# Kernel optimization log

Measured on AMD Instinct MI355X. Metric: run time of the kernel, lower is better.

## Reference

```python
import jax, jax.numpy as jnp
import numpy as np

H = 16  # heads


def setup_inputs() -> dict:
    key = jax.random.key(0)
    ks = jax.random.split(key, 10)
    B, S, M = 4, 2048, 1024
    scale = 1.0 / np.sqrt(M)
    return {
        "x": jax.random.normal(ks[0], (B, S, M), dtype=jnp.float32),
        "mask": jax.random.uniform(ks[1], (B, 1, S, S), dtype=jnp.float32),
        "Wq": jax.random.normal(ks[2], (M, M), dtype=jnp.float32) * scale,
        "bq": jax.random.normal(ks[3], (M,), dtype=jnp.float32) * scale,
        "Wk": jax.random.normal(ks[4], (M, M), dtype=jnp.float32) * scale,
        "bk": jax.random.normal(ks[5], (M,), dtype=jnp.float32) * scale,
        "Wv": jax.random.normal(ks[6], (M, M), dtype=jnp.float32) * scale,
        "bv": jax.random.normal(ks[7], (M,), dtype=jnp.float32) * scale,
        "Wo": jax.random.normal(ks[8], (M, M), dtype=jnp.float32) * scale,
        "bo": jax.random.normal(ks[9], (M,), dtype=jnp.float32) * scale,
    }


def reference(x, mask, Wq, bq, Wk, bk, Wv, bv, Wo, bo):
    B, S, M = x.shape
    dk = M // H
    # QKV projections (torch Linear: x @ W.T + b), then split heads -> [B,H,S,dk]
    q = (x @ Wq.T + bq).reshape(B, S, H, dk).transpose(0, 2, 1, 3)
    k = (x @ Wk.T + bk).reshape(B, S, H, dk).transpose(0, 2, 1, 3)
    v = (x @ Wv.T + bv).reshape(B, S, H, dk).transpose(0, 2, 1, 3)
    # scores: [B,H,S,S], multiplicative mask (non-standard!) then softmax
    scores = jnp.einsum("bhqd,bhkd->bhqk", q, k) / jnp.sqrt(jnp.float32(dk))
    scores = scores * mask  # mask broadcasts over heads
    attn = jax.nn.softmax(scores, axis=-1)
    # dropout is identity in eval/reference mode
    out = jnp.einsum("bhqk,bhkd->bhqd", attn, v)  # [B,H,S,dk]
    concat = out.transpose(0, 2, 1, 3).reshape(B, S, M)
    return concat @ Wo.T + bo
```

## Files before the change

### kernel.cpp

```cpp
#include <hip/hip_runtime.h>

typedef __attribute__((ext_vector_type(8))) short s16x8;
typedef __attribute__((ext_vector_type(4))) short s16x4;
typedef __attribute__((ext_vector_type(4))) float f32x4;
typedef __attribute__((ext_vector_type(16))) float f32x16;
typedef __attribute__((ext_vector_type(2))) unsigned int u32x2;

#define DEV static __device__ __forceinline__

DEV void gload_lds16(const void* g, void* l) {
  __builtin_amdgcn_global_load_lds(
      (const __attribute__((address_space(1))) void*)g,
      (__attribute__((address_space(3))) void*)l, 16, 0, 0);
}

DEV unsigned short f2bf(float f) {
  unsigned int u = __float_as_uint(f);
  u = (u + 0x7fffu + ((u >> 16) & 1u)) >> 16;
  return (unsigned short)u;
}

DEV unsigned pk2(float lo, float hi) {
  unsigned r;
  asm("v_cvt_pk_bf16_f32 %0, %1, %2" : "=v"(r) : "v"(lo), "v"(hi));
  return r;
}

DEV float exp2_fast(float x) {
  float r;
  asm("v_exp_f32 %0, %1" : "=v"(r) : "v"(x));
  return r;
}

DEV void cvt8(const float* __restrict__ in, unsigned short* __restrict__ out, int i) {
  float4 a = *(const float4*)(in + i);
  float4 b = *(const float4*)(in + i + 4);
  union { s16x8 v; unsigned short u[8]; } o;
  o.u[0] = f2bf(a.x); o.u[1] = f2bf(a.y); o.u[2] = f2bf(a.z); o.u[3] = f2bf(a.w);
  o.u[4] = f2bf(b.x); o.u[5] = f2bf(b.y); o.u[6] = f2bf(b.z); o.u[7] = f2bf(b.w);
  *(s16x8*)(out + i) = o.v;
}

__global__ __launch_bounds__(256) void k_cvt_all(
    const float* __restrict__ x, const float* __restrict__ Wq,
    const float* __restrict__ Wk, const float* __restrict__ Wv,
    const float* __restrict__ Wo, unsigned short* __restrict__ xb,
    unsigned short* __restrict__ wcat) {
  const int bid = blockIdx.x;
  if (bid < 4096) {
    cvt8(x, xb, (bid * 256 + threadIdx.x) * 8);
  } else {
    const int id = bid - 4096;
    const int sel = id >> 9;
    const float* in = (sel == 0) ? Wq : (sel == 1) ? Wk : (sel == 2) ? Wv : Wo;
    cvt8(in, wcat + sel * 1048576, ((id & 511) * 256 + threadIdx.x) * 8);
  }
}

__global__ __launch_bounds__(256) void k_gemm_qkv(
    const unsigned short* __restrict__ A, const unsigned short* __restrict__ Bcat,
    const float* __restrict__ bq, const float* __restrict__ bk,
    const float* __restrict__ bv,
    unsigned short* __restrict__ outQK, unsigned short* __restrict__ vtw) {
  constexpr int K = 1024;
  constexpr float QSC = 0.125f * 1.44269504f;
  __shared__ unsigned short As[128 * 64];
  __shared__ unsigned short Bs[128 * 64];

  const int lin = blockIdx.x;
  const int logical = (lin & 7) * 192 + (lin >> 3);
  const int nb = logical % 24;
  const int mb = logical / 24;
  const int m0 = mb * 128;
  const int n0 = nb * 128;
  const int z = n0 >> 10;

  const int tid = threadIdx.x;
  const int lane = tid & 63;
  const int l15 = lane & 15, g = lane >> 4;
  const int w = tid >> 6;
  const int wr = w >> 1, wc = w & 1;

  const int sr = tid >> 3;
  const int sc = tid & 7;

  f32x4 acc[4][4] = {};

  for (int kt = 0; kt < K / 64; ++kt) {
#pragma unroll
    for (int i = 0; i < 4; ++i) {
      const int row = i * 32 + sr;
      gload_lds16(A + (size_t)(m0 + row) * K + kt * 64 + ((sc ^ (row & 7)) * 8),
                  (void*)(As + i * 2048 + tid * 8));
      gload_lds16(Bcat + (size_t)(n0 + row) * K + kt * 64 + ((sc ^ (row & 7)) * 8),
                  (void*)(Bs + i * 2048 + tid * 8));
    }
    __syncthreads();
#pragma unroll
    for (int ks = 0; ks < 2; ++ks) {
      s16x8 af[4], bf[4];
#pragma unroll
      for (int i = 0; i < 4; ++i) {
        const int ra = wr * 64 + i * 16 + l15;
        af[i] = *(const s16x8*)(As + ra * 64 + (((ks * 4 + g) ^ (ra & 7)) * 8));
        const int rb = wc * 64 + i * 16 + l15;
        bf[i] = *(const s16x8*)(Bs + rb * 64 + (((ks * 4 + g) ^ (rb & 7)) * 8));
      }
#pragma unroll
      for (int i = 0; i < 4; ++i)
#pragma unroll
        for (int j = 0; j < 4; ++j)
          acc[i][j] = __builtin_amdgcn_mfma_f32_16x16x32_bf16(af[i], bf[j], acc[i][j], 0, 0, 0);
    }
    __syncthreads();
  }

  const float* bias = (z == 0) ? bq : (z == 1) ? bk : bv;
  const float osc = (z == 0) ? QSC : 1.0f;
#pragma unroll
  for (int j = 0; j < 4; ++j) {
    const int gcol = n0 + wc * 64 + j * 16 + l15;
    const int col = gcol & 1023;
    const float bvv = bias[col];
    const int h = col >> 6, d = col & 63;
#pragma unroll
    for (int i = 0; i < 4; ++i) {
      const int grow0 = m0 + wr * 64 + i * 16 + g * 4;
      const int bb = grow0 >> 11, s0 = grow0 & 2047;
      if (z < 2) {
        unsigned short* outp = outQK + (size_t)z * 8388608;
#pragma unroll
        for (int r = 0; r < 4; ++r)
          outp[(((size_t)(bb * 16 + h) * 2048 + (s0 + r)) << 6) + d] =
              f2bf((acc[i][j][r] + bvv) * osc);
      } else {
        union { s16x4 v; unsigned short u[4]; } pk;
#pragma unroll
        for (int r = 0; r < 4; ++r) pk.u[r] = f2bf(acc[i][j][r] + bvv);
        *(s16x4*)(vtw + (((size_t)(bb * 16 + h)) << 17) + (size_t)d * 2048 + s0) = pk.v;
      }
    }
  }
}

__global__ __launch_bounds__(256) void k_gemm_o(
    const unsigned short* __restrict__ A, const unsigned short* __restrict__ Bw,
    const float* __restrict__ bias, float* __restrict__ outp) {
  constexpr int K = 1024;
  __shared__ unsigned short As[128 * 64];
  __shared__ unsigned short Bs[64 * 64];

  const int lin = blockIdx.x;
  const int logical = (lin & 7) * 128 + (lin >> 3);
  const int nb = logical & 15;
  const int mb = logical >> 4;
  const int m0 = mb * 128, n0 = nb * 64;

  const int tid = threadIdx.x;
  const int lane = tid & 63;
  const int l15 = lane & 15, g = lane >> 4;
  const int w = tid >> 6;
  const int wr = w >> 1, wc = w & 1;

  const int sr = tid >> 3;
  const int sc = tid & 7;

  f32x4 acc[4][2] = {};

  for (int kt = 0; kt < K / 64; ++kt) {
#pragma unroll
    for (int i = 0; i < 4; ++i) {
      const int row = i * 32 + sr;
      gload_lds16(A + (size_t)(m0 + row) * K + kt * 64 + ((sc ^ (row & 7)) * 8),
                  (void*)(As + i * 2048 + tid * 8));
    }
#pragma unroll
    for (int i = 0; i < 2; ++i) {
      const int row = i * 32 + sr;
      gload_lds16(Bw + (size_t)(n0 + row) * K + kt * 64 + ((sc ^ (row & 7)) * 8),
                  (void*)(Bs + i * 2048 + tid * 8));
    }
    __syncthreads();
#pragma unroll
    for (int ks = 0; ks < 2; ++ks) {
      s16x8 af[4], bf[2];
#pragma unroll
      for (int mi = 0; mi < 4; ++mi) {
        const int ra = wr * 64 + mi * 16 + l15;
        af[mi] = *(const s16x8*)(As + ra * 64 + (((ks * 4 + g) ^ (ra & 7)) * 8));
      }
#pragma unroll
      for (int nj = 0; nj < 2; ++nj) {
        const int rb = wc * 32 + nj * 16 + l15;
        bf[nj] = *(const s16x8*)(Bs + rb * 64 + (((ks * 4 + g) ^ (rb & 7)) * 8));
      }
#pragma unroll
      for (int mi = 0; mi < 4; ++mi)
#pragma unroll
        for (int nj = 0; nj < 2; ++nj)
          acc[mi][nj] =
              __builtin_amdgcn_mfma_f32_16x16x32_bf16(af[mi], bf[nj], acc[mi][nj], 0, 0, 0);
    }
    __syncthreads();
  }

#pragma unroll
  for (int nj = 0; nj < 2; ++nj) {
    const int gcol = n0 + wc * 32 + nj * 16 + l15;
    const float bv = bias[gcol];
#pragma unroll
    for (int mi = 0; mi < 4; ++mi)
#pragma unroll
      for (int r = 0; r < 4; ++r) {
        const int grow = m0 + wr * 64 + mi * 16 + g * 4 + r;
        outp[(size_t)grow * 1024 + gcol] = acc[mi][nj][r] + bv;
      }
  }
}

__global__ __launch_bounds__(256) void k_attn3(
    const unsigned short* __restrict__ q, const unsigned short* __restrict__ k,
    const unsigned short* __restrict__ vt, const float* __restrict__ mask,
    unsigned short* __restrict__ concat) {
  __shared__ unsigned short Ks[2][64 * 64];
  __shared__ unsigned short Vs[2][64 * 64];

  const int tid = threadIdx.x;
  const int lane = tid & 63;
  const int w = tid >> 6;
  const int l31 = lane & 31;
  const int hh = lane >> 5;

  const int lin = blockIdx.x + 16 * (blockIdx.y + 16 * blockIdx.z);
  const int logical = (lin & 7) * 128 + (lin >> 3);
  const int h = logical & 15;
  const int qt = (logical >> 4) & 15;
  const int b = logical >> 8;

  const size_t bhO = (size_t)(b * 16 + h) * (2048 * 64);
  const unsigned short* kb = k + bhO;
  const unsigned short* vb = vt + bhO;
  const int q0 = qt * 128;
  const int qc = w * 32 + l31;
  const int qg = q0 + qc;

  s16x8 qf[4];
  {
    const unsigned short* qp = q + bhO + (size_t)qg * 64 + hh * 8;
#pragma unroll
    for (int kd = 0; kd < 4; ++kd) qf[kd] = *(const s16x8*)(qp + kd * 16);
  }

  const float* mlane = mask + (size_t)b * 4194304 + (size_t)qg * 2048 + hh * 4;

  float m_r = -3.0e38f, l_r = 0.f;
  f32x16 oacc[2] = {};

  const int sr = tid >> 3;
  const int sc = tid & 7;

#define STAGE(BUF, T_)                                                                \
  {                                                                                   \
    const int kv0s = (T_)*64;                                                         \
    _Pragma("unroll") for (int i = 0; i < 2; ++i) {                                   \
      const int row = i * 32 + sr;                                                    \
      const int sz = (sc ^ (row & 7)) * 8;                                            \
      gload_lds16(kb + (size_t)(kv0s + row) * 64 + sz,                                \
                  (void*)(Ks[BUF] + i * 2048 + tid * 8));                             \
      gload_lds16(vb + (size_t)row * 2048 + kv0s + sz,                                \
                  (void*)(Vs[BUF] + i * 2048 + tid * 8));                             \
    }                                                                                 \
  }

  STAGE(0, 0)
  __syncthreads();

  for (int tt = 0; tt < 16; ++tt) {
#pragma unroll
    for (int half = 0; half < 2; ++half) {
      const int t = tt * 2 + half;

      float4 mvf[8];
#pragma unroll
      for (int f = 0; f < 2; ++f)
#pragma unroll
        for (int rq = 0; rq < 4; ++rq)
          mvf[f * 4 + rq] = *(const float4*)(mlane + f * 32 + rq * 8);
      mlane += 64;

      if (t < 31) STAGE(half ^ 1, t + 1)

      f32x16 sacc[2] = {};
      __builtin_amdgcn_s_setprio(1);
#pragma unroll
      for (int f = 0; f < 2; ++f) {
        const int rk = f * 32 + l31;
        const unsigned short* Kr = Ks[half] + rk * 64;
        const int swb = rk & 7;
#pragma unroll
        for (int kd = 0; kd < 4; ++kd) {
          const s16x8 kf = *(const s16x8*)(Kr + (((kd * 2 + hh) ^ swb) * 8));
          sacc[f] = __builtin_amdgcn_mfma_f32_32x32x16_bf16(kf, qf[kd], sacc[f], 0, 0, 0);
        }
      }
      __builtin_amdgcn_s_setprio(0);

      float p[32];
#pragma unroll
      for (int f = 0; f < 2; ++f)
#pragma unroll
        for (int rq = 0; rq < 4; ++rq)
#pragma unroll
          for (int j = 0; j < 4; ++j)
            p[f * 16 + rq * 4 + j] = sacc[f][rq * 4 + j] * mvf[f * 4 + rq][j];

      float a3[11];
#pragma unroll
      for (int i = 0; i < 10; ++i)
        a3[i] = fmaxf(fmaxf(p[3 * i], p[3 * i + 1]), p[3 * i + 2]);
      a3[10] = fmaxf(p[30], p[31]);
      const float b0 = fmaxf(fmaxf(a3[0], a3[1]), a3[2]);
      const float b1 = fmaxf(fmaxf(a3[3], a3[4]), a3[5]);
      const float b2 = fmaxf(fmaxf(a3[6], a3[7]), a3[8]);
      const float b3 = fmaxf(a3[9], a3[10]);
      float tm = fmaxf(fmaxf(fmaxf(b0, b1), b2), b3);
      tm = fmaxf(tm, __shfl_xor(tm, 32, 64));

      if (__any(tm > m_r + 11.5f)) {
        const float mn = fmaxf(m_r, tm);
        const float rs = exp2_fast(m_r - mn);
        m_r = mn;
        l_r *= rs;
#pragma unroll
        for (int df = 0; df < 2; ++df)
#pragma unroll
          for (int r = 0; r < 16; ++r) oacc[df][r] *= rs;
      }
      float ps = 0.f;
#pragma unroll
      for (int n = 0; n < 32; ++n) {
        p[n] = exp2_fast(p[n] - m_r);
        ps += p[n];
      }
      ps += __shfl_xor(ps, 32, 64);
      l_r += ps;

#pragma unroll
      for (int ks = 0; ks < 4; ++ks) {
        const int pb = ks * 8;
        const unsigned X0 = pk2(p[pb + 0], p[pb + 1]);
        const unsigned X1 = pk2(p[pb + 2], p[pb + 3]);
        const unsigned Y0 = pk2(p[pb + 4], p[pb + 5]);
        const unsigned Y1 = pk2(p[pb + 6], p[pb + 7]);
        const u32x2 r0 = __builtin_amdgcn_permlane32_swap(X0, Y0, false, false);
        const u32x2 r1 = __builtin_amdgcn_permlane32_swap(X1, Y1, false, false);
        union { s16x8 v; unsigned u[4]; } pf;
        pf.u[0] = r0.x; pf.u[1] = r1.x; pf.u[2] = r0.y; pf.u[3] = r1.y;
        __builtin_amdgcn_s_setprio(1);
#pragma unroll
        for (int df = 0; df < 2; ++df) {
          const int rv = df * 32 + l31;
          const s16x8 vf =
              *(const s16x8*)(Vs[half] + rv * 64 + (((ks * 2 + hh) ^ (rv & 7)) * 8));
          oacc[df] = __builtin_amdgcn_mfma_f32_32x32x16_bf16(vf, pf.v, oacc[df], 0, 0, 0);
        }
        __builtin_amdgcn_s_setprio(0);
      }
      __syncthreads();
    }
  }
#undef STAGE

  const float inv = 1.0f / l_r;
  unsigned short* cb = concat + ((size_t)b * 2048 + qg) * 1024 + h * 64;
#pragma unroll
  for (int df = 0; df < 2; ++df)
#pragma unroll
    for (int r = 0; r < 16; r += 2) {
      const int d = df * 32 + (r & 3) + 8 * (r >> 2) + 4 * hh;
      const unsigned u = (unsigned)f2bf(oacc[df][r] * inv) |
                         ((unsigned)f2bf(oacc[df][r + 1] * inv) << 16);
      *(unsigned*)(cb + d) = u;
    }
}

extern "C" void kernel_launch(void* const* d_in, const int* in_sizes, int n_in,
                              void* d_out, int out_size, void* d_ws, size_t ws_size,
                              hipStream_t stream) {
  const float* x    = (const float*)d_in[0];
  const float* mask = (const float*)d_in[1];
  const float* Wq   = (const float*)d_in[2];
  const float* bq   = (const float*)d_in[3];
  const float* Wk   = (const float*)d_in[4];
  const float* bk   = (const float*)d_in[5];
  const float* Wv   = (const float*)d_in[6];
  const float* bv   = (const float*)d_in[7];
  const float* Wo   = (const float*)d_in[8];
  const float* bo   = (const float*)d_in[9];

  char* ws = (char*)d_ws;
  unsigned short* xb    = (unsigned short*)(ws);
  unsigned short* wcat  = (unsigned short*)(ws + (size_t)16777216);
  unsigned short* wob   = wcat + 3 * 1048576;
  unsigned short* qw    = (unsigned short*)(ws + (size_t)25165824);
  unsigned short* kw    = qw + 8388608;
  unsigned short* vtw   = (unsigned short*)(ws + (size_t)58720256);
  unsigned short* cw    = xb;

  k_cvt_all<<<dim3(6144), dim3(256), 0, stream>>>(x, Wq, Wk, Wv, Wo, xb, wcat);
  k_gemm_qkv<<<dim3(1536), dim3(256), 0, stream>>>(xb, wcat, bq, bk, bv, qw, vtw);
  k_attn3<<<dim3(16, 16, 4), dim3(256), 0, stream>>>(qw, kw, vtw, mask, cw);
  k_gemm_o<<<dim3(1024), dim3(256), 0, stream>>>(cw, wob, bo, (float*)d_out);
}
```

Before: 256.8 us.

## Pre-convert mask to bf16 in MFMA fragment layout before attention

A new pre-pass kernel converts the fp32 attention mask to bf16. It stores it in a slab laid out to match each lane's MFMA score fragment, so each lane reads its mask values as contiguous 16-byte vectors. The attention kernel, which re-reads the mask once per head, now loads half as many bytes with fully coalesced accesses instead of strided float4 loads. The cost is an extra kernel pass that reads the whole fp32 mask and writes 32 MB of workspace, plus reduced mask precision from rounding to bf16.

```diff
diff --git a/kernel.cpp b/kernel.cpp
--- a/kernel.cpp
+++ b/kernel.cpp
@@ -19,6 +19,8 @@
   u = (u + 0x7fffu + ((u >> 16) & 1u)) >> 16;
   return (unsigned short)u;
 }
+
+DEV float bf2f(unsigned short u) { return __uint_as_float((unsigned)u << 16); }
 
 DEV unsigned pk2(float lo, float hi) {
   unsigned r;
@@ -57,6 +59,36 @@
   }
 }
 
+__global__ __launch_bounds__(256) void k_maskP(const float* __restrict__ mask,
+                                               unsigned short* __restrict__ slab) {
+  __shared__ unsigned short Mt[128 * 68];
+  const int tid = threadIdx.x;
+  const int t = blockIdx.x, qt = blockIdx.y, b = blockIdx.z;
+  const float* src = mask + (size_t)b * 4194304 + (size_t)qt * 128 * 2048 + t * 64;
+#pragma unroll
+  for (int it = 0; it < 8; ++it) {
+    const int c = it * 256 + tid;
+    const int row = c >> 4, kc = c & 15;
+    const float4 v = *(const float4*)(src + (size_t)row * 2048 + kc * 4);
+    unsigned short* d = Mt + row * 68 + kc * 4;
+    d[0] = f2bf(v.x); d[1] = f2bf(v.y); d[2] = f2bf(v.z); d[3] = f2bf(v.w);
+  }
+  __syncthreads();
+  unsigned short* dst = slab + ((((size_t)b * 16 + qt) * 32 + t) * 8192);
+#pragma unroll
+  for (int it = 0; it < 4; ++it) {
+    const int c = it * 256 + tid;
+    const int w = c >> 8, i2 = (c >> 6) & 3, ln = c & 63;
+    const int qrow = w * 32 + (ln & 31);
+    const int kbase = 32 * (i2 >> 1) + 16 * (i2 & 1) + 4 * (ln >> 5);
+    union { s16x8 v; unsigned short u[8]; } o;
+#pragma unroll
+    for (int e = 0; e < 8; ++e)
+      o.u[e] = Mt[qrow * 68 + kbase + 8 * (e >> 2) + (e & 3)];
+    *(s16x8*)(dst + c * 8) = o.v;
+  }
+}
+
 __global__ __launch_bounds__(256) void k_gemm_qkv(
     const unsigned short* __restrict__ A, const unsigned short* __restrict__ Bcat,
     const float* __restrict__ bq, const float* __restrict__ bk,
@@ -220,7 +252,7 @@
 
 __global__ __launch_bounds__(256) void k_attn3(
     const unsigned short* __restrict__ q, const unsigned short* __restrict__ k,
-    const unsigned short* __restrict__ vt, const float* __restrict__ mask,
+    const unsigned short* __restrict__ vt, const unsigned short* __restrict__ slab,
     unsigned short* __restrict__ concat) {
   __shared__ unsigned short Ks[2][64 * 64];
   __shared__ unsigned short Vs[2][64 * 64];
@@ -251,7 +283,8 @@
     for (int kd = 0; kd < 4; ++kd) qf[kd] = *(const s16x8*)(qp + kd * 16);
   }
 
-  const float* mlane = mask + (size_t)b * 4194304 + (size_t)qg * 2048 + hh * 4;
+  const unsigned short* mp =
+      slab + ((((size_t)b * 16 + qt) * 32) * 8192) + ((size_t)(w * 4) * 64 + lane) * 8;
 
   float m_r = -3.0e38f, l_r = 0.f;
   f32x16 oacc[2] = {};
@@ -280,13 +313,10 @@
     for (int half = 0; half < 2; ++half) {
       const int t = tt * 2 + half;
 
-      float4 mvf[8];
-#pragma unroll
-      for (int f = 0; f < 2; ++f)
-#pragma unroll
-        for (int rq = 0; rq < 4; ++rq)
-          mvf[f * 4 + rq] = *(const float4*)(mlane + f * 32 + rq * 8);
-      mlane += 64;
+      s16x8 mv[4];
+#pragma unroll
+      for (int i2 = 0; i2 < 4; ++i2) mv[i2] = *(const s16x8*)(mp + i2 * 512);
+      mp += 8192;
 
       if (t < 31) STAGE(half ^ 1, t + 1)
 
@@ -309,10 +339,11 @@
 #pragma unroll
       for (int f = 0; f < 2; ++f)
 #pragma unroll
-        for (int rq = 0; rq < 4; ++rq)
-#pragma unroll
-          for (int j = 0; j < 4; ++j)
-            p[f * 16 + rq * 4 + j] = sacc[f][rq * 4 + j] * mvf[f * 4 + rq][j];
+        for (int kk = 0; kk < 2; ++kk)
+#pragma unroll
+          for (int e = 0; e < 8; ++e)
+            p[f * 16 + kk * 8 + e] =
+                sacc[f][kk * 8 + e] * bf2f((unsigned short)mv[f * 2 + kk][e]);
 
       float a3[11];
 #pragma unroll
@@ -405,10 +436,12 @@
   unsigned short* qw    = (unsigned short*)(ws + (size_t)25165824);
   unsigned short* kw    = qw + 8388608;
   unsigned short* vtw   = (unsigned short*)(ws + (size_t)58720256);
+  unsigned short* slab  = (unsigned short*)(ws + (size_t)75497472);
   unsigned short* cw    = xb;
 
   k_cvt_all<<<dim3(6144), dim3(256), 0, stream>>>(x, Wq, Wk, Wv, Wo, xb, wcat);
+  k_maskP<<<dim3(32, 16, 4), dim3(256), 0, stream>>>(mask, slab);
   k_gemm_qkv<<<dim3(1536), dim3(256), 0, stream>>>(xb, wcat, bq, bk, bv, qw, vtw);
-  k_attn3<<<dim3(16, 16, 4), dim3(256), 0, stream>>>(qw, kw, vtw, mask, cw);
+  k_attn3<<<dim3(16, 16, 4), dim3(256), 0, stream>>>(qw, kw, vtw, slab, cw);
   k_gemm_o<<<dim3(1024), dim3(256), 0, stream>>>(cw, wob, bo, (float*)d_out);
 }
```

New measurement: 241.2 us. 1.06x faster.
